# Performance work log

Measured on AMD Instinct MI355X. Metric: run time of the kernel, lower is better.

Reference implementation:

```python
import jax, jax.numpy as jnp
import numpy as np


def setup_inputs() -> dict:
    key = jax.random.key(0)
    k0, k1, k2, k3 = jax.random.split(key, 4)
    B, M, H, K, OUT = 256, 64, 64, 128, 256
    x0 = jax.random.normal(k0, (B, M, K), dtype=jnp.float32)
    xl = jax.random.normal(k1, (B, H, K), dtype=jnp.float32)
    # Conv1d(in_channels=M*H, out_channels=OUT, kernel_size=1) params
    fan_in = M * H  # kernel_size=1
    bound = 1.0 / np.sqrt(fan_in)
    W = jax.random.uniform(k2, (OUT, M * H, 1), dtype=jnp.float32, minval=-bound, maxval=bound)
    b = jax.random.uniform(k3, (OUT,), dtype=jnp.float32, minval=-bound, maxval=bound)
    return {"x0": x0, "xl": xl, "k": K, "W": W, "b": b}


def reference(x0, xl, k, W, b):
    # x0: [B, m, k_emb], xl: [B, h, k_emb]
    # Fused equivalent of the per-column loop: for each embedding column i,
    # matmul(xl[:,:,i:i+1], x0[:,:,i:i+1]^T) -> [B,h,m]; stacked over k -> [B,h,m,k]
    fmap = jnp.einsum('bhk,bmk->bhmk', xl, x0)
    B = x0.shape[0]
    h, m = xl.shape[1], x0.shape[1]
    fmap = fmap.reshape(B, h * m, k)  # [B, h*m, k]
    # 1x1 Conv1d == GEMM over channel dim
    out = jnp.einsum('bck,oc->bok', fmap, W[:, :, 0]) + b[None, :, None]
    return out
```

## Files before the change

kernel.cpp:

```cpp
#include <hip/hip_runtime.h>
#include <hip/hip_bf16.h>
#include <stdint.h>


typedef __attribute__((ext_vector_type(8)))  short    short8;
typedef __attribute__((ext_vector_type(8)))  _Float16 f16x8;
typedef __attribute__((ext_vector_type(2)))  _Float16 h2v;
typedef __attribute__((ext_vector_type(16))) float    f32x16;

#define B_SZ   256
#define K_SZ   128
#define OUT_SZ 256
#define C_SZ   4096
#define NH     64

__device__ __forceinline__ uint32_t pack_f16(float a, float b) {
    union { h2v h; uint32_t u; } v;
    v.h = (h2v){(_Float16)a, (_Float16)b};
    return v.u;
}

__device__ __forceinline__ void load_lds_16(const void* g, void* l) {
    __builtin_amdgcn_global_load_lds(
        (const __attribute__((address_space(1))) unsigned int*)g,
        (__attribute__((address_space(3))) unsigned int*)l,
        16, 0, 0);
}

__global__ void convert_W_tiled(const float* __restrict__ W, short* __restrict__ Wb) {
    int t = blockIdx.x * blockDim.x + threadIdx.x;
    int lane = t & 63;
    int sub  = t >> 6;
    int cb16 = sub & 255;
    int got  = sub >> 8;
    int o = got * 32 + (lane & 31);
    int c = cb16 * 16 + (lane >> 5) * 8;
    const float* p = W + (size_t)o * C_SZ + c;
    float4 w0 = *(const float4*)p;
    float4 w1 = *(const float4*)(p + 4);
    union { short8 s; uint32_t u[4]; } cc;
    cc.u[0] = pack_f16(w0.x, w0.y);
    cc.u[1] = pack_f16(w0.z, w0.w);
    cc.u[2] = pack_f16(w1.x, w1.y);
    cc.u[3] = pack_f16(w1.z, w1.w);
    *(short8*)(Wb + (size_t)t * 8) = cc.s;
}

template<bool USE_WS>
__global__ __launch_bounds__(256, 2)
void cin_main(const float* __restrict__ x0, const float* __restrict__ xl,
              const float* __restrict__ Wf, const short* __restrict__ Wb,
              const float* __restrict__ bias, float* __restrict__ out) {
    __shared__ short    Wlds[2 * 4 * 4096];
    __shared__ uint32_t xls[NH * 64];

    const int b     = blockIdx.y;
    const int khalf = blockIdx.x;
    const int kb    = khalf * 64;
    const int tid   = threadIdx.x;
    const int lane  = tid & 63;
    const int wave  = tid >> 6;
    const int l31   = lane & 31;
    const int hi    = lane >> 5;

    {
        const int h    = tid >> 2;
        const int koff = (tid & 3) * 16;
        const float4* src = (const float4*)(xl + (size_t)b * (NH * K_SZ)
                                            + h * K_SZ + kb + koff);
        uint32_t* dst = &xls[h * 64 + koff];
#pragma unroll
        for (int i = 0; i < 4; ++i) {
            float4 v = src[i];
            dst[4 * i + 0] = pack_f16(v.x, v.x);
            dst[4 * i + 1] = pack_f16(v.y, v.y);
            dst[4 * i + 2] = pack_f16(v.z, v.z);
            dst[4 * i + 3] = pack_f16(v.w, v.w);
        }
    }

    union X0P { f16x8 v; h2v h[4]; uint32_t u[4]; } x0p[4][2];
    {
        const float* x0b = x0 + (size_t)b * (64 * K_SZ);
#pragma unroll
        for (int cb = 0; cb < 4; ++cb)
#pragma unroll
            for (int nt = 0; nt < 2; ++nt)
#pragma unroll
                for (int t2 = 0; t2 < 4; ++t2) {
                    const int m0 = cb * 16 + hi * 8 + 2 * t2;
                    const int cc = kb + nt * 32 + l31;
                    x0p[cb][nt].u[t2] = pack_f16(x0b[m0 * K_SZ + cc],
                                                 x0b[(m0 + 1) * K_SZ + cc]);
                }
    }

    const short* wsrc0 = Wb + ((size_t)(2 * wave) * 256) * 512 + lane * 8;
    const short* wsrc1 = Wb + ((size_t)(2 * wave + 1) * 256) * 512 + lane * 8;
    const float* wfrow0 = Wf + (size_t)(2 * wave * 32 + l31) * C_SZ + hi * 8;
    const float* wfrow1 = wfrow0 + (size_t)32 * C_SZ;

    auto wlb = [&](int buf) { return Wlds + buf * 16384 + wave * 4096; };

    auto stage = [&](int buf, int h) {
        short* d = wlb(buf);
        if (USE_WS) {
            const short* s0 = wsrc0 + (size_t)(4 * h) * 512;
            const short* s1 = wsrc1 + (size_t)(4 * h) * 512;
#pragma unroll
            for (int cb = 0; cb < 4; ++cb)
                load_lds_16(s0 + cb * 512, d + cb * 512);
#pragma unroll
            for (int cb = 0; cb < 4; ++cb)
                load_lds_16(s1 + cb * 512, d + 2048 + cb * 512);
        } else {
#pragma unroll
            for (int ot = 0; ot < 2; ++ot) {
                const float* wf = ot ? wfrow1 : wfrow0;
#pragma unroll
                for (int cb = 0; cb < 4; ++cb) {
                    const float* p = wf + h * 64 + cb * 16;
                    float4 w0 = *(const float4*)p;
                    float4 w1 = *(const float4*)(p + 4);
                    union { short8 s; uint32_t u[4]; } cc;
                    cc.u[0] = pack_f16(w0.x, w0.y);
                    cc.u[1] = pack_f16(w0.z, w0.w);
                    cc.u[2] = pack_f16(w1.x, w1.y);
                    cc.u[3] = pack_f16(w1.z, w1.w);
                    *(short8*)(d + ot * 2048 + cb * 512 + lane * 8) = cc.s;
                }
            }
        }
    };

    f32x16 acc[2][2];
#pragma unroll
    for (int ot = 0; ot < 2; ++ot)
#pragma unroll
        for (int nt = 0; nt < 2; ++nt)
#pragma unroll
            for (int r = 0; r < 16; ++r) acc[ot][nt][r] = 0.f;

    stage(0, 0);
    stage(1, 1);
    __syncthreads();

    for (int h = 0; h < NH; ++h) {
        if (USE_WS) asm volatile("s_waitcnt vmcnt(8)" ::: "memory");

        const short* wb2 = wlb(h & 1) + lane * 8;
        f16x8 af[2][4];
#pragma unroll
        for (int ot = 0; ot < 2; ++ot)
#pragma unroll
            for (int cb = 0; cb < 4; ++cb)
                af[ot][cb] = *(const f16x8*)(wb2 + ot * 2048 + cb * 512);

        h2v xld0, xld1;
        { union { uint32_t u; h2v h; } t0, t1;
          t0.u = xls[h * 64 + 0 * 32 + l31];
          t1.u = xls[h * 64 + 1 * 32 + l31];
          xld0 = t0.h; xld1 = t1.h; }

        __builtin_amdgcn_s_setprio(1);
#pragma unroll
        for (int cb = 0; cb < 4; ++cb) {
            union X0P b0, b1;
#pragma unroll
            for (int t2 = 0; t2 < 4; ++t2) {
                b0.h[t2] = xld0 * x0p[cb][0].h[t2];
                b1.h[t2] = xld1 * x0p[cb][1].h[t2];
            }
            acc[0][0] = __builtin_amdgcn_mfma_f32_32x32x16_f16(af[0][cb], b0.v, acc[0][0], 0, 0, 0);
            acc[0][1] = __builtin_amdgcn_mfma_f32_32x32x16_f16(af[0][cb], b1.v, acc[0][1], 0, 0, 0);
            acc[1][0] = __builtin_amdgcn_mfma_f32_32x32x16_f16(af[1][cb], b0.v, acc[1][0], 0, 0, 0);
            acc[1][1] = __builtin_amdgcn_mfma_f32_32x32x16_f16(af[1][cb], b1.v, acc[1][1], 0, 0, 0);
        }
        __builtin_amdgcn_s_setprio(0);

        asm volatile("s_waitcnt lgkmcnt(0)" ::: "memory");
        stage(h & 1, (h + 2) & (NH - 1));
    }

    float* outb = out + (size_t)b * (OUT_SZ * K_SZ);
#pragma unroll
    for (int ot = 0; ot < 2; ++ot) {
        const int obase = (2 * wave + ot) * 32;
#pragma unroll
        for (int r = 0; r < 16; ++r) {
            const int orow = obase + (r & 3) + 8 * (r >> 2) + 4 * hi;
            const float bv = bias[orow];
#pragma unroll
            for (int nt = 0; nt < 2; ++nt)
                outb[orow * K_SZ + kb + nt * 32 + l31] = acc[ot][nt][r] + bv;
        }
    }
}

extern "C" void kernel_launch(void* const* d_in, const int* in_sizes, int n_in,
                              void* d_out, int out_size, void* d_ws, size_t ws_size,
                              hipStream_t stream) {
    const float* x0   = (const float*)d_in[0];
    const float* xl   = (const float*)d_in[1];
    const float* W    = (const float*)d_in[3];
    const float* bias = (const float*)d_in[4];
    float* out = (float*)d_out;

    const size_t w_bytes = (size_t)OUT_SZ * C_SZ * sizeof(short);
    short* Wb = (short*)d_ws;

    if (ws_size >= w_bytes) {
        convert_W_tiled<<<dim3(512), dim3(256), 0, stream>>>(W, Wb);
        cin_main<true><<<dim3(2, B_SZ), dim3(256), 0, stream>>>(x0, xl, W, Wb, bias, out);
    } else {
        cin_main<false><<<dim3(2, B_SZ), dim3(256), 0, stream>>>(x0, xl, W, Wb, bias, out);
    }
}
```

Baseline: 91.39 us.

## Load W fragments directly into registers and split output channels across more blocks

Drops the LDS double-buffered W staging and instead loads each wave's W fragments straight from global memory into registers, ping-ponging between two fragment sets. The grid doubles to split output channels into halves, so each wave owns one 32-row output tile and the occupancy hint rises to 3. Each block starts its h loop at an offset derived from the batch index to spread W reads. The cost is that the x0/xl setup work is repeated per output half and global loads now sit directly in the compute loop with no explicit wait control.

Result: faster. 85.27 us (-6.7%).

```diff
diff --git a/kernel.cpp b/kernel.cpp
--- a/kernel.cpp
+++ b/kernel.cpp
@@ -20,13 +20,6 @@
     return v.u;
 }
 
-__device__ __forceinline__ void load_lds_16(const void* g, void* l) {
-    __builtin_amdgcn_global_load_lds(
-        (const __attribute__((address_space(1))) unsigned int*)g,
-        (__attribute__((address_space(3))) unsigned int*)l,
-        16, 0, 0);
-}
-
 __global__ void convert_W_tiled(const float* __restrict__ W, short* __restrict__ Wb) {
     int t = blockIdx.x * blockDim.x + threadIdx.x;
     int lane = t & 63;
@@ -47,19 +40,21 @@
 }
 
 template<bool USE_WS>
-__global__ __launch_bounds__(256, 2)
+__global__ __launch_bounds__(256, 3)
 void cin_main(const float* __restrict__ x0, const float* __restrict__ xl,
               const float* __restrict__ Wf, const short* __restrict__ Wb,
               const float* __restrict__ bias, float* __restrict__ out) {
-    __shared__ short    Wlds[2 * 4 * 4096];
     __shared__ uint32_t xls[NH * 64];
 
     const int b     = blockIdx.y;
-    const int khalf = blockIdx.x;
+    const int bx    = blockIdx.x;
+    const int ohalf = bx >> 1;
+    const int khalf = bx & 1;
     const int kb    = khalf * 64;
     const int tid   = threadIdx.x;
     const int lane  = tid & 63;
     const int wave  = tid >> 6;
+    const int got   = ohalf * 4 + wave;
     const int l31   = lane & 31;
     const int hi    = lane >> 5;
 
@@ -95,105 +90,82 @@
                 }
     }
 
-    const short* wsrc0 = Wb + ((size_t)(2 * wave) * 256) * 512 + lane * 8;
-    const short* wsrc1 = Wb + ((size_t)(2 * wave + 1) * 256) * 512 + lane * 8;
-    const float* wfrow0 = Wf + (size_t)(2 * wave * 32 + l31) * C_SZ + hi * 8;
-    const float* wfrow1 = wfrow0 + (size_t)32 * C_SZ;
+    const short* wsrc  = Wb + ((size_t)got * 256) * 512 + (size_t)lane * 8;
+    const float* wfrow = Wf + (size_t)(got * 32 + l31) * C_SZ + hi * 8;
+    const int h0 = b & (NH - 1);
 
-    auto wlb = [&](int buf) { return Wlds + buf * 16384 + wave * 4096; };
-
-    auto stage = [&](int buf, int h) {
-        short* d = wlb(buf);
+    auto LOAD_AF = [&](f16x8* dst, int hh) {
         if (USE_WS) {
-            const short* s0 = wsrc0 + (size_t)(4 * h) * 512;
-            const short* s1 = wsrc1 + (size_t)(4 * h) * 512;
+            const short* s0 = wsrc + (size_t)(4 * hh) * 512;
 #pragma unroll
             for (int cb = 0; cb < 4; ++cb)
-                load_lds_16(s0 + cb * 512, d + cb * 512);
-#pragma unroll
-            for (int cb = 0; cb < 4; ++cb)
-                load_lds_16(s1 + cb * 512, d + 2048 + cb * 512);
+                dst[cb] = *(const f16x8*)(s0 + cb * 512);
         } else {
 #pragma unroll
-            for (int ot = 0; ot < 2; ++ot) {
-                const float* wf = ot ? wfrow1 : wfrow0;
-#pragma unroll
-                for (int cb = 0; cb < 4; ++cb) {
-                    const float* p = wf + h * 64 + cb * 16;
-                    float4 w0 = *(const float4*)p;
-                    float4 w1 = *(const float4*)(p + 4);
-                    union { short8 s; uint32_t u[4]; } cc;
-                    cc.u[0] = pack_f16(w0.x, w0.y);
-                    cc.u[1] = pack_f16(w0.z, w0.w);
-                    cc.u[2] = pack_f16(w1.x, w1.y);
-                    cc.u[3] = pack_f16(w1.z, w1.w);
-                    *(short8*)(d + ot * 2048 + cb * 512 + lane * 8) = cc.s;
-                }
+            for (int cb = 0; cb < 4; ++cb) {
+                const float* p = wfrow + hh * 64 + cb * 16;
+                float4 w0 = *(const float4*)p;
+                float4 w1 = *(const float4*)(p + 4);
+                union { f16x8 v; uint32_t u[4]; } cc;
+                cc.u[0] = pack_f16(w0.x, w0.y);
+                cc.u[1] = pack_f16(w0.z, w0.w);
+                cc.u[2] = pack_f16(w1.x, w1.y);
+                cc.u[3] = pack_f16(w1.z, w1.w);
+                dst[cb] = cc.v;
             }
         }
     };
 
-    f32x16 acc[2][2];
+    f32x16 acc[2];
 #pragma unroll
-    for (int ot = 0; ot < 2; ++ot)
+    for (int nt = 0; nt < 2; ++nt)
 #pragma unroll
-        for (int nt = 0; nt < 2; ++nt)
-#pragma unroll
-            for (int r = 0; r < 16; ++r) acc[ot][nt][r] = 0.f;
+        for (int r = 0; r < 16; ++r) acc[nt][r] = 0.f;
 
-    stage(0, 0);
-    stage(1, 1);
+    f16x8 afA[4], afB[4];
+    LOAD_AF(afA, h0);
+    LOAD_AF(afB, (h0 + 1) & (NH - 1));
     __syncthreads();
 
-    for (int h = 0; h < NH; ++h) {
-        if (USE_WS) asm volatile("s_waitcnt vmcnt(8)" ::: "memory");
+#define COMPUTE(AF, HH)                                                              \
+    do {                                                                             \
+        const int h_ = (HH) & (NH - 1);                                              \
+        h2v xld0, xld1;                                                              \
+        { union { uint32_t u; h2v h; } t0, t1;                                       \
+          t0.u = xls[h_ * 64 + 0 * 32 + l31];                                        \
+          t1.u = xls[h_ * 64 + 1 * 32 + l31];                                        \
+          xld0 = t0.h; xld1 = t1.h; }                                                \
+        __builtin_amdgcn_s_setprio(1);                                               \
+        _Pragma("unroll")                                                            \
+        for (int cb = 0; cb < 4; ++cb) {                                             \
+            union X0P b0, b1;                                                        \
+            _Pragma("unroll")                                                        \
+            for (int t2 = 0; t2 < 4; ++t2) {                                         \
+                b0.h[t2] = xld0 * x0p[cb][0].h[t2];                                  \
+                b1.h[t2] = xld1 * x0p[cb][1].h[t2];                                  \
+            }                                                                        \
+            acc[0] = __builtin_amdgcn_mfma_f32_32x32x16_f16(AF[cb], b0.v, acc[0], 0, 0, 0); \
+            acc[1] = __builtin_amdgcn_mfma_f32_32x32x16_f16(AF[cb], b1.v, acc[1], 0, 0, 0); \
+        }                                                                            \
+        __builtin_amdgcn_s_setprio(0);                                               \
+    } while (0)
 
-        const short* wb2 = wlb(h & 1) + lane * 8;
-        f16x8 af[2][4];
-#pragma unroll
-        for (int ot = 0; ot < 2; ++ot)
-#pragma unroll
-            for (int cb = 0; cb < 4; ++cb)
-                af[ot][cb] = *(const f16x8*)(wb2 + ot * 2048 + cb * 512);
-
-        h2v xld0, xld1;
-        { union { uint32_t u; h2v h; } t0, t1;
-          t0.u = xls[h * 64 + 0 * 32 + l31];
-          t1.u = xls[h * 64 + 1 * 32 + l31];
-          xld0 = t0.h; xld1 = t1.h; }
-
-        __builtin_amdgcn_s_setprio(1);
-#pragma unroll
-        for (int cb = 0; cb < 4; ++cb) {
-            union X0P b0, b1;
-#pragma unroll
-            for (int t2 = 0; t2 < 4; ++t2) {
-                b0.h[t2] = xld0 * x0p[cb][0].h[t2];
-                b1.h[t2] = xld1 * x0p[cb][1].h[t2];
-            }
-            acc[0][0] = __builtin_amdgcn_mfma_f32_32x32x16_f16(af[0][cb], b0.v, acc[0][0], 0, 0, 0);
-            acc[0][1] = __builtin_amdgcn_mfma_f32_32x32x16_f16(af[0][cb], b1.v, acc[0][1], 0, 0, 0);
-            acc[1][0] = __builtin_amdgcn_mfma_f32_32x32x16_f16(af[1][cb], b0.v, acc[1][0], 0, 0, 0);
-            acc[1][1] = __builtin_amdgcn_mfma_f32_32x32x16_f16(af[1][cb], b1.v, acc[1][1], 0, 0, 0);
-        }
-        __builtin_amdgcn_s_setprio(0);
-
-        asm volatile("s_waitcnt lgkmcnt(0)" ::: "memory");
-        stage(h & 1, (h + 2) & (NH - 1));
+    for (int i = 0; i < NH; i += 2) {
+        COMPUTE(afA, h0 + i);
+        LOAD_AF(afA, (h0 + i + 2) & (NH - 1));
+        COMPUTE(afB, h0 + i + 1);
+        LOAD_AF(afB, (h0 + i + 3) & (NH - 1));
     }
+#undef COMPUTE
 
     float* outb = out + (size_t)b * (OUT_SZ * K_SZ);
 #pragma unroll
-    for (int ot = 0; ot < 2; ++ot) {
-        const int obase = (2 * wave + ot) * 32;
+    for (int r = 0; r < 16; ++r) {
+        const int orow = got * 32 + (r & 3) + 8 * (r >> 2) + 4 * hi;
+        const float bv = bias[orow];
 #pragma unroll
-        for (int r = 0; r < 16; ++r) {
-            const int orow = obase + (r & 3) + 8 * (r >> 2) + 4 * hi;
-            const float bv = bias[orow];
-#pragma unroll
-            for (int nt = 0; nt < 2; ++nt)
-                outb[orow * K_SZ + kb + nt * 32 + l31] = acc[ot][nt][r] + bv;
-        }
+        for (int nt = 0; nt < 2; ++nt)
+            outb[orow * K_SZ + kb + nt * 32 + l31] = acc[nt][r] + bv;
     }
 }
 
@@ -211,8 +183,8 @@
 
     if (ws_size >= w_bytes) {
         convert_W_tiled<<<dim3(512), dim3(256), 0, stream>>>(W, Wb);
-        cin_main<true><<<dim3(2, B_SZ), dim3(256), 0, stream>>>(x0, xl, W, Wb, bias, out);
+        cin_main<true><<<dim3(4, B_SZ), dim3(256), 0, stream>>>(x0, xl, W, Wb, bias, out);
     } else {
-        cin_main<false><<<dim3(2, B_SZ), dim3(256), 0, stream>>>(x0, xl, W, Wb, bias, out);
+        cin_main<false><<<dim3(4, B_SZ), dim3(256), 0, stream>>>(x0, xl, W, Wb, bias, out);
     }
 }
```
